# Optimization experiments

Hardware: AMD Instinct MI355X
Metric: run time of the kernel (lower is better)

## Reference

```python
import jax, jax.numpy as jnp
import numpy as np

EMBED = 1024
HEADS = 16
HIDDEN = 4 * EMBED
EPS = 1e-5


def layer_norm(x, g, b):
    mu = jnp.mean(x, axis=-1, keepdims=True)
    var = jnp.var(x, axis=-1, keepdims=True)
    return (x - mu) * jax.lax.rsqrt(var + EPS) * g + b


def setup_inputs() -> dict:
    key = jax.random.key(0)
    ks = jax.random.split(key, 8)
    s = EMBED ** -0.5
    return {
        "x": jax.random.normal(ks[0], (4, 2048, EMBED), dtype=jnp.float32),
        "ln1_g": jnp.ones((EMBED,), jnp.float32),
        "ln1_b": jnp.zeros((EMBED,), jnp.float32),
        "qkv_w": jax.random.normal(ks[1], (3 * EMBED, EMBED), jnp.float32) * s,
        "out_w": jax.random.normal(ks[2], (EMBED, EMBED), jnp.float32) * s,
        "out_b": jnp.zeros((EMBED,), jnp.float32),
        "ln2_g": jnp.ones((EMBED,), jnp.float32),
        "ln2_b": jnp.zeros((EMBED,), jnp.float32),
        "fc1_w": jax.random.normal(ks[3], (HIDDEN, EMBED), jnp.float32) * s,
        "fc1_b": jnp.zeros((HIDDEN,), jnp.float32),
        "fc2_w": jax.random.normal(ks[4], (EMBED, HIDDEN), jnp.float32) * (HIDDEN ** -0.5),
        "fc2_b": jnp.zeros((EMBED,), jnp.float32),
    }


def reference(x, ln1_g, ln1_b, qkv_w, out_w, out_b, ln2_g, ln2_b, fc1_w, fc1_b, fc2_w, fc2_b):
    B, N, C = x.shape
    hd = C // HEADS
    # --- attention (pre-LN); note: NO 1/sqrt(d) scaling, matching the source ---
    h = layer_norm(x, ln1_g, ln1_b)
    qkv = h @ qkv_w.T                                  # [B,N,3C]
    qkv = qkv.reshape(B, N, 3, HEADS, hd).transpose(2, 0, 3, 1, 4)
    q, k, v = qkv[0], qkv[1], qkv[2]                   # [B,H,N,hd]
    attn = jax.nn.softmax(jnp.einsum("bhqd,bhkd->bhqk", q, k), axis=-1)
    o = jnp.einsum("bhqk,bhkd->bhqd", attn, v)
    o = o.transpose(0, 2, 1, 3).reshape(B, N, C)
    x = x + o @ out_w.T + out_b
    # --- MLP (exact erf GELU, matching nn.GELU default) ---
    h = layer_norm(x, ln2_g, ln2_b)
    h = jax.nn.gelu(h @ fc1_w.T + fc1_b, approximate=False)
    x = x + h @ fc2_w.T + fc2_b
    return x
```

## Files before the change

### kernel.cpp

```cpp
#include <hip/hip_runtime.h>
#include <cstdint>


using short8 = __attribute__((ext_vector_type(8))) short;
using f32x4  = __attribute__((ext_vector_type(4))) float;
using f32x16 = __attribute__((ext_vector_type(16))) float;

#define EMBED  1024
#define HIDDEN 4096
#define SEQ    2048
#define NTOK   8192
#define LOG2E  1.4426950408889634f

__device__ __forceinline__ ushort f2bf(float x) {
  union { float f; uint32_t u; } v; v.f = x;
  uint32_t r = v.u + 0x7fffu + ((v.u >> 16) & 1u);
  return (ushort)(r >> 16);
}

__device__ __forceinline__ uint32_t pkbf(float lo, float hi) {
  uint32_t r;
  asm("v_cvt_pk_bf16_f32 %0, %1, %2" : "=v"(r) : "v"(lo), "v"(hi));
  return r;
}

__device__ __forceinline__ void gload16(const void* g, void* l) {
  __builtin_amdgcn_global_load_lds((__attribute__((address_space(1))) void*)(g),
                                   (__attribute__((address_space(3))) void*)(l), 16, 0, 0);
}

template<int N> __device__ __forceinline__ void vwait() {
  asm volatile("s_waitcnt vmcnt(%0)" :: "n"(N) : "memory");
}
__device__ __forceinline__ void lgkm0() {
  asm volatile("s_waitcnt lgkmcnt(0)" ::: "memory");
}
__device__ __forceinline__ void fence_bar() {
  asm volatile("" ::: "memory");
  __builtin_amdgcn_s_barrier();
  asm volatile("" ::: "memory");
}

__device__ __forceinline__ f32x4 mfma16(short8 a, short8 b, f32x4 c) {
  return __builtin_amdgcn_mfma_f32_16x16x32_bf16(a, b, c, 0, 0, 0);
}
__device__ __forceinline__ f32x16 mfma32(short8 a, short8 b, f32x16 c) {
  return __builtin_amdgcn_mfma_f32_32x32x16_bf16(a, b, c, 0, 0, 0);
}
__device__ __forceinline__ f32x16 zero16() {
  f32x16 z = {0.f,0.f,0.f,0.f,0.f,0.f,0.f,0.f,0.f,0.f,0.f,0.f,0.f,0.f,0.f,0.f};
  return z;
}

__global__ __launch_bounds__(256) void cvt4_kernel(const float* __restrict__ s0, ushort* __restrict__ d0, int n0,
                                                   const float* __restrict__ s1, ushort* __restrict__ d1, int n1,
                                                   const float* __restrict__ s2, ushort* __restrict__ d2, int n2,
                                                   const float* __restrict__ s3, ushort* __restrict__ d3, int n3) {
  const int total = n0 + n1 + n2 + n3;
  for (int i = blockIdx.x * 256 + threadIdx.x; i < total; i += gridDim.x * 256) {
    const float* s; ushort* d; int j = i;
    if (j < n0) { s = s0; d = d0; }
    else {
      j -= n0;
      if (j < n1) { s = s1; d = d1; }
      else {
        j -= n1;
        if (j < n2) { s = s2; d = d2; }
        else { j -= n2; s = s3; d = d3; }
      }
    }
    const float4 v = reinterpret_cast<const float4*>(s)[j];
    ushort4 o; o.x = f2bf(v.x); o.y = f2bf(v.y); o.z = f2bf(v.z); o.w = f2bf(v.w);
    reinterpret_cast<ushort4*>(d)[j] = o;
  }
}

__global__ __launch_bounds__(256) void ln_kernel(const float* __restrict__ x,
                                                 const float* __restrict__ g,
                                                 const float* __restrict__ b,
                                                 ushort* __restrict__ out) {
  const int row = blockIdx.x, tid = threadIdx.x;
  const float4 xv = reinterpret_cast<const float4*>(x + (size_t)row * EMBED)[tid];
  float s  = xv.x + xv.y + xv.z + xv.w;
  float s2 = xv.x*xv.x + xv.y*xv.y + xv.z*xv.z + xv.w*xv.w;
  #pragma unroll
  for (int off = 32; off >= 1; off >>= 1) { s += __shfl_xor(s, off); s2 += __shfl_xor(s2, off); }
  __shared__ float ps[4], ps2[4];
  if ((tid & 63) == 0) { ps[tid >> 6] = s; ps2[tid >> 6] = s2; }
  __syncthreads();
  s  = ps[0] + ps[1] + ps[2] + ps[3];
  s2 = ps2[0] + ps2[1] + ps2[2] + ps2[3];
  const float mu  = s * (1.f / EMBED);
  const float var = s2 * (1.f / EMBED) - mu * mu;
  const float rs  = rsqrtf(var + 1e-5f);
  const float4 gv = reinterpret_cast<const float4*>(g)[tid];
  const float4 bv = reinterpret_cast<const float4*>(b)[tid];
  ushort4 o;
  o.x = f2bf((xv.x - mu) * rs * gv.x + bv.x);
  o.y = f2bf((xv.y - mu) * rs * gv.y + bv.y);
  o.z = f2bf((xv.z - mu) * rs * gv.z + bv.z);
  o.w = f2bf((xv.w - mu) * rs * gv.w + bv.w);
  reinterpret_cast<ushort4*>(out + (size_t)row * EMBED)[tid] = o;
}

template<int EPI, bool SQ>
__global__ __launch_bounds__(512) void gemm256(const ushort* __restrict__ A,
                                               const ushort* __restrict__ B,
                                               const float* __restrict__ bias,
                                               const float* __restrict__ res,
                                               ushort* __restrict__ outb,
                                               float* __restrict__ outf,
                                               int M, int N, int K, int gx) {
  constexpr int BN   = SQ ? 256 : 128;
  constexpr int MP   = SQ ? 8 : 4;
  constexpr int NPH  = SQ ? 2 : 1;
  constexpr int LPT  = SQ ? 4 : 3;
  constexpr int NB   = LPT - 2;
  constexpr int ABUF = 256 * 32;
  constexpr int BBUF = BN * 32;
  __shared__ ushort lds[4][ABUF + BBUF];

  const int nwg = gridDim.x;
  const int b0  = blockIdx.x;
  const int p = b0 & 7, li = b0 >> 3;
  int mt, nt;
  if ((gx & 7) == 0) {
    const int g = gx >> 3;
    mt = p * g + (li % g);
    nt = li / g;
  } else {
    const int g = (nwg / gx) >> 3;
    nt = p * g + (li % g);
    mt = li / g;
  }
  const int m0 = mt * 256;
  const int n0 = nt * BN;

  const int tid = threadIdx.x, lane = tid & 63, wave = tid >> 6;
  const int wm = (SQ ? (wave >> 2) : (wave >> 1)) * (MP * 16);
  const int wn = (SQ ? (wave & 3) : (wave & 1)) * 64;
  const int l15 = lane & 15, l4 = lane >> 4;
  const int NT = K >> 5;

  const ushort* aSrc[2];
  const ushort* bSrc[NB];
  #pragma unroll
  for (int rd = 0; rd < 2; ++rd) {
    const int slot = rd * 512 + tid;
    const int r = slot >> 2;
    const int cs = (slot & 3) ^ ((r >> 1) & 3);
    aSrc[rd] = A + (size_t)(m0 + r) * K + cs * 8;
  }
  #pragma unroll
  for (int rd = 0; rd < NB; ++rd) {
    const int slot = rd * 512 + tid;
    const int r = slot >> 2;
    const int cs = (slot & 3) ^ ((r >> 1) & 3);
    bSrc[rd] = B + (size_t)(n0 + r) * K + cs * 8;
  }
  auto stageA = [&](int buf, int rd) { gload16(aSrc[rd], &lds[buf][(rd * 512 + tid) * 8]); };
  auto stageB = [&](int buf, int rd) { gload16(bSrc[rd], &lds[buf][ABUF + (rd * 512 + tid) * 8]); };
  auto advance = [&]() {
    #pragma unroll
    for (int rd = 0; rd < 2; ++rd) aSrc[rd] += 32;
    #pragma unroll
    for (int rd = 0; rd < NB; ++rd) bSrc[rd] += 32;
  };

  #pragma unroll
  for (int t = 0; t < 3; ++t) {
    stageA(t, 0); stageA(t, 1);
    #pragma unroll
    for (int rd = 0; rd < NB; ++rd) stageB(t, rd);
    advance();
  }
  vwait<2 * LPT>();
  fence_bar();

  f32x4 acc[MP][4] = {};

  auto doTile = [&](int q, bool st, int wsel) {
    const ushort* bA = &lds[q][0];
    const ushort* bB = &lds[q][ABUF];
    const int sbuf = (q + 3) & 3;
    short8 bf[4];
    #pragma unroll
    for (int j = 0; j < 4; ++j) {
      const int rb = wn + j * 16 + l15;
      bf[j] = *reinterpret_cast<const short8*>(&bB[rb * 32 + ((l4 ^ ((rb >> 1) & 3)) * 8)]);
    }
    #pragma unroll
    for (int ph = 0; ph < NPH; ++ph) {
      short8 af[4];
      #pragma unroll
      for (int i = 0; i < 4; ++i) {
        const int ra = wm + (ph * 4 + i) * 16 + l15;
        af[i] = *reinterpret_cast<const short8*>(&bA[ra * 32 + ((l4 ^ ((ra >> 1) & 3)) * 8)]);
      }
      if (st) {
        if constexpr (SQ) {
          if (ph == 0) { stageA(sbuf, 0); stageA(sbuf, 1); }
          else         { stageB(sbuf, 0); stageB(sbuf, 1); }
        } else {
          stageA(sbuf, 0); stageA(sbuf, 1); stageB(sbuf, 0);
        }
      }
      fence_bar();
      __builtin_amdgcn_s_setprio(1);
      #pragma unroll
      for (int i = 0; i < 4; ++i)
        #pragma unroll
        for (int j = 0; j < 4; ++j)
          acc[ph * 4 + i][j] = mfma16(af[i], bf[j], acc[ph * 4 + i][j]);
      __builtin_amdgcn_s_setprio(0);
      if (ph == NPH - 1) {
        if (st) advance();
        if (wsel == 0)      vwait<2 * LPT>();
        else if (wsel == 1) vwait<LPT>();
        else if (wsel == 2) vwait<0>();
      }
      fence_bar();
    }
  };

  for (int u0 = 0; u0 < NT - 4; u0 += 4) {
    doTile(0, true, 0); doTile(1, true, 0); doTile(2, true, 0); doTile(3, true, 0);
  }
  doTile(0, true, 0); doTile(1, false, 1); doTile(2, false, 2); doTile(3, false, 3);

  #pragma unroll
  for (int i = 0; i < MP; ++i)
    #pragma unroll
    for (int j = 0; j < 4; ++j)
      #pragma unroll
      for (int r = 0; r < 4; ++r) {
        const int row = m0 + wm + i * 16 + l4 * 4 + r;
        const int col = n0 + wn + j * 16 + l15;
        const size_t idx = (size_t)row * N + col;
        float v = acc[i][j][r];
        if constexpr (EPI == 0) {
          outb[idx] = f2bf(v);
        } else if constexpr (EPI == 1) {
          outf[idx] = v + bias[col] + res[idx];
        } else if constexpr (EPI == 2) {
          v += bias[col];
          v = 0.5f * v * (1.f + erff(v * 0.70710678118654752f));
          outb[idx] = f2bf(v);
        } else {
          outb[idx] = f2bf((col < 1024) ? v * LOG2E : v);
        }
      }
}

#define KVB 64
#define NTT (SEQ / KVB)

__global__ __launch_bounds__(512, 4) void attn_kernel(const ushort* __restrict__ qk,
                                                      const ushort* __restrict__ vt,
                                                      ushort* __restrict__ outp) {
  const int tid = threadIdx.x, lane = tid & 63, wq = tid >> 6;
  const int hi = lane >> 5, lo = lane & 31;
  const int b = blockIdx.x >> 4, h = blockIdx.x & 15;
  const int q0 = blockIdx.y * 256;

  __shared__ ushort sK[2][64 * 64];
  __shared__ ushort sVt[2][64 * 64];
  __shared__ float sBc[8][32];

  short8 qf[4];
  #pragma unroll
  for (int kc = 0; kc < 4; ++kc)
    qf[kc] = *reinterpret_cast<const short8*>(
        qk + (size_t)(b * SEQ + q0 + wq * 32 + lo) * 2048 + h * 64 + kc * 16 + hi * 8);

  auto STAGE = [&](int bb, int kt) {
    const int r = tid >> 3;
    const int c = (tid & 7) ^ (r & 7);
    gload16(qk + (size_t)(b * SEQ + kt + r) * 2048 + 1024 + h * 64 + c * 8,
            &sK[bb][wq * 64 * 8]);
    gload16(vt + (size_t)(h * 64 + r) * 8192 + b * SEQ + kt + c * 8,
            &sVt[bb][wq * 64 * 8]);
  };

  f32x16 acc[2];
  acc[0] = zero16(); acc[1] = zero16();
  float mst = -1e30f, lst = 0.f;

  STAGE(0, 0);
  for (int t = 0; t < NTT; ++t) {
    const int cur = t & 1;
    __syncthreads();
    if (t + 1 < NTT) STAGE(cur ^ 1, (t + 1) * KVB);

    short8 kf[2][4];
    #pragma unroll
    for (int kvb = 0; kvb < 2; ++kvb)
      #pragma unroll
      for (int kc = 0; kc < 4; ++kc) {
        const int row = kvb * 32 + lo, ch = kc * 2 + hi;
        kf[kvb][kc] = *reinterpret_cast<const short8*>(
            &sK[cur][(row * 8 + (ch ^ (row & 7))) * 8]);
      }

    f32x16 st[2];
    #pragma unroll
    for (int kvb = 0; kvb < 2; ++kvb) {
      f32x16 tq = zero16();
      tq = mfma32(kf[kvb][0], qf[0], tq);
      tq = mfma32(kf[kvb][1], qf[1], tq);
      tq = mfma32(kf[kvb][2], qf[2], tq);
      tq = mfma32(kf[kvb][3], qf[3], tq);
      st[kvb] = tq;
    }
    f32x16 mm;
    #pragma unroll
    for (int r = 0; r < 16; ++r) mm[r] = fmaxf(st[0][r], st[1][r]);
    float pm = fmaxf(fmaxf(mm[0], mm[1]), mm[2]);
    pm = fmaxf(fmaxf(pm, mm[3]), mm[4]);
    pm = fmaxf(fmaxf(pm, mm[5]), mm[6]);
    pm = fmaxf(fmaxf(pm, mm[7]), mm[8]);
    pm = fmaxf(fmaxf(pm, mm[9]), mm[10]);
    pm = fmaxf(fmaxf(pm, mm[11]), mm[12]);
    pm = fmaxf(fmaxf(pm, mm[13]), mm[14]);
    pm = fmaxf(pm, mm[15]);
    pm = fmaxf(pm, __shfl_xor(pm, 32));
    if (__any(pm > mst + 11.54f)) {
      const float mn = fmaxf(mst, pm);
      const float al = __builtin_amdgcn_exp2f(mst - mn);
      mst = mn; lst *= al;
      sBc[wq][lo] = al;
      lgkm0();
      #pragma unroll
      for (int g = 0; g < 4; ++g) {
        const f32x4 a4 = *reinterpret_cast<const f32x4*>(&sBc[wq][g * 8 + hi * 4]);
        #pragma unroll
        for (int j = 0; j < 4; ++j) {
          acc[0][g * 4 + j] *= a4[j];
          acc[1][g * 4 + j] *= a4[j];
        }
      }
    }
    #pragma unroll
    for (int kvb = 0; kvb < 2; ++kvb)
      #pragma unroll
      for (int r = 0; r < 16; ++r)
        st[kvb][r] = __builtin_amdgcn_exp2f(st[kvb][r] - mst);
    {
      const f32x16 sv = st[0] + st[1];
      float sum = ((sv[0] + sv[1]) + (sv[2] + sv[3])) + ((sv[4] + sv[5]) + (sv[6] + sv[7]))
                + ((sv[8] + sv[9]) + (sv[10] + sv[11])) + ((sv[12] + sv[13]) + (sv[14] + sv[15]));
      sum += __shfl_xor(sum, 32);
      lst += sum;
    }
    short8 pa[4];
    #pragma unroll
    for (int kvb = 0; kvb < 2; ++kvb)
      #pragma unroll
      for (int f = 0; f < 2; ++f) {
        uint32_t wa = pkbf(st[kvb][f * 8 + 0], st[kvb][f * 8 + 1]);
        uint32_t wb = pkbf(st[kvb][f * 8 + 2], st[kvb][f * 8 + 3]);
        uint32_t wc = pkbf(st[kvb][f * 8 + 4], st[kvb][f * 8 + 5]);
        uint32_t wd = pkbf(st[kvb][f * 8 + 6], st[kvb][f * 8 + 7]);
        asm volatile("v_permlane32_swap_b32 %0, %1" : "+v"(wa), "+v"(wc));
        asm volatile("v_permlane32_swap_b32 %0, %1" : "+v"(wb), "+v"(wd));
        union { uint32_t w[4]; short8 v; } u;
        u.w[0] = wa; u.w[1] = wb; u.w[2] = wc; u.w[3] = wd;
        pa[kvb * 2 + f] = u.v;
      }

    #pragma unroll
    for (int db = 0; db < 2; ++db) {
      short8 vb[4];
      #pragma unroll
      for (int k4 = 0; k4 < 4; ++k4) {
        const int row = db * 32 + lo, ch = k4 * 2 + hi;
        vb[k4] = *reinterpret_cast<const short8*>(
            &sVt[cur][(row * 8 + (ch ^ (row & 7))) * 8]);
      }
      acc[db] = mfma32(pa[0], vb[0], acc[db]);
      acc[db] = mfma32(pa[1], vb[1], acc[db]);
      acc[db] = mfma32(pa[2], vb[2], acc[db]);
      acc[db] = mfma32(pa[3], vb[3], acc[db]);
    }
  }

  sBc[wq][lo] = 1.f / lst;
  lgkm0();
  #pragma unroll
  for (int g = 0; g < 4; ++g) {
    const f32x4 r4 = *reinterpret_cast<const f32x4*>(&sBc[wq][g * 8 + hi * 4]);
    #pragma unroll
    for (int j = 0; j < 4; ++j) {
      const int qrow = q0 + wq * 32 + g * 8 + hi * 4 + j;
      #pragma unroll
      for (int db = 0; db < 2; ++db)
        outp[(size_t)(b * SEQ + qrow) * EMBED + h * 64 + db * 32 + lo] =
            f2bf(acc[db][g * 4 + j] * r4[j]);
    }
  }
}

extern "C" void kernel_launch(void* const* d_in, const int* in_sizes, int n_in,
                              void* d_out, int out_size, void* d_ws, size_t ws_size,
                              hipStream_t stream) {
  const float* x     = (const float*)d_in[0];
  const float* ln1_g = (const float*)d_in[1];
  const float* ln1_b = (const float*)d_in[2];
  const float* qkv_w = (const float*)d_in[3];
  const float* out_w = (const float*)d_in[4];
  const float* out_b = (const float*)d_in[5];
  const float* ln2_g = (const float*)d_in[6];
  const float* ln2_b = (const float*)d_in[7];
  const float* fc1_w = (const float*)d_in[8];
  const float* fc1_b = (const float*)d_in[9];
  const float* fc2_w = (const float*)d_in[10];
  const float* fc2_b = (const float*)d_in[11];
  float* out = (float*)d_out;
  char* ws = (char*)d_ws;

  ushort* qkvw = (ushort*)(ws);
  ushort* outw = (ushort*)(ws + 6291456);
  ushort* fc1w = (ushort*)(ws + 8388608);
  ushort* fc2w = (ushort*)(ws + 16777216);
  float*  x1   = (float*) (ws + 25165824);
  ushort* hbuf = (ushort*)(ws + 58720256);
  ushort* qkbuf= (ushort*)(ws + 75497472);
  ushort* vtbuf= (ushort*)(ws + 109051904);
  ushort* obuf = (ushort*)(ws + 125829120);
  ushort* gbuf = qkbuf;

  cvt4_kernel<<<2048, 256, 0, stream>>>(qkv_w, qkvw, 3 * EMBED * EMBED / 4,
                                        out_w, outw, EMBED * EMBED / 4,
                                        fc1_w, fc1w, HIDDEN * EMBED / 4,
                                        fc2_w, fc2w, EMBED * HIDDEN / 4);

  ln_kernel<<<NTOK, 256, 0, stream>>>(x, ln1_g, ln1_b, hbuf);
  gemm256<3, true><<<256, 512, 0, stream>>>(hbuf, qkvw, nullptr, nullptr,
                                            qkbuf, nullptr, NTOK, 2 * EMBED, EMBED, 32);
  gemm256<0, false><<<256, 512, 0, stream>>>(qkvw + 2048 * 1024, hbuf, nullptr, nullptr,
                                             vtbuf, nullptr, EMBED, NTOK, EMBED, 4);
  attn_kernel<<<dim3(64, 8), 512, 0, stream>>>(qkbuf, vtbuf, obuf);
  gemm256<1, false><<<256, 512, 0, stream>>>(obuf, outw, out_b, x,
                                             nullptr, x1, NTOK, EMBED, EMBED, 32);
  ln_kernel<<<NTOK, 256, 0, stream>>>(x1, ln2_g, ln2_b, hbuf);
  gemm256<2, true><<<512, 512, 0, stream>>>(hbuf, fc1w, fc1_b, nullptr,
                                            gbuf, nullptr, NTOK, HIDDEN, EMBED, 32);
  gemm256<1, false><<<256, 512, 0, stream>>>(gbuf, fc2w, fc2_b, x1,
                                             nullptr, out, NTOK, EMBED, HIDDEN, 32);
}
```

Measured before the change: 379.9 us.

## Switch GEMM to double-buffered LDS and fold LOG2E into Q weights

The GEMM pipeline drops from a 4-stage LDS ring (three tiles in flight, loads issued mid-MFMA) to two buffers, where the next tile's loads are issued after the MFMAs and a barrier. Swizzled LDS offsets are now computed once outside the loop. The LOG2E scaling of Q moves from the QKV GEMM epilogue into the weight-conversion kernel. This halves LDS use, which may allow more resident workgroups, but exposes more global-load latency because less is prefetched and compute overlaps loads less.

```diff
diff --git a/kernel.cpp b/kernel.cpp
--- a/kernel.cpp
+++ b/kernel.cpp
@@ -58,8 +58,8 @@
                                                    const float* __restrict__ s3, ushort* __restrict__ d3, int n3) {
   const int total = n0 + n1 + n2 + n3;
   for (int i = blockIdx.x * 256 + threadIdx.x; i < total; i += gridDim.x * 256) {
-    const float* s; ushort* d; int j = i;
-    if (j < n0) { s = s0; d = d0; }
+    const float* s; ushort* d; int j = i; float sc = 1.f;
+    if (j < n0) { s = s0; d = d0; if (j < (EMBED * EMBED / 4)) sc = LOG2E; }
     else {
       j -= n0;
       if (j < n1) { s = s1; d = d1; }
@@ -70,7 +70,8 @@
       }
     }
     const float4 v = reinterpret_cast<const float4*>(s)[j];
-    ushort4 o; o.x = f2bf(v.x); o.y = f2bf(v.y); o.z = f2bf(v.z); o.w = f2bf(v.w);
+    ushort4 o; o.x = f2bf(v.x * sc); o.y = f2bf(v.y * sc);
+    o.z = f2bf(v.z * sc); o.w = f2bf(v.w * sc);
     reinterpret_cast<ushort4*>(d)[j] = o;
   }
 }
@@ -118,7 +119,7 @@
   constexpr int NB   = LPT - 2;
   constexpr int ABUF = 256 * 32;
   constexpr int BBUF = BN * 32;
-  __shared__ ushort lds[4][ABUF + BBUF];
+  __shared__ ushort lds[2][ABUF + BBUF];
 
   const int nwg = gridDim.x;
   const int b0  = blockIdx.x;
@@ -167,14 +168,26 @@
     for (int rd = 0; rd < NB; ++rd) bSrc[rd] += 32;
   };
 
-  #pragma unroll
-  for (int t = 0; t < 3; ++t) {
+  int aOff[MP], bOff[4];
+  #pragma unroll
+  for (int i = 0; i < MP; ++i) {
+    const int ra = wm + i * 16 + l15;
+    aOff[i] = ra * 32 + ((l4 ^ ((ra >> 1) & 3)) * 8);
+  }
+  #pragma unroll
+  for (int j = 0; j < 4; ++j) {
+    const int rb = wn + j * 16 + l15;
+    bOff[j] = rb * 32 + ((l4 ^ ((rb >> 1) & 3)) * 8);
+  }
+
+  #pragma unroll
+  for (int t = 0; t < 2; ++t) {
     stageA(t, 0); stageA(t, 1);
     #pragma unroll
     for (int rd = 0; rd < NB; ++rd) stageB(t, rd);
     advance();
   }
-  vwait<2 * LPT>();
+  vwait<LPT>();
   fence_bar();
 
   f32x4 acc[MP][4] = {};
@@ -182,30 +195,16 @@
   auto doTile = [&](int q, bool st, int wsel) {
     const ushort* bA = &lds[q][0];
     const ushort* bB = &lds[q][ABUF];
-    const int sbuf = (q + 3) & 3;
     short8 bf[4];
     #pragma unroll
-    for (int j = 0; j < 4; ++j) {
-      const int rb = wn + j * 16 + l15;
-      bf[j] = *reinterpret_cast<const short8*>(&bB[rb * 32 + ((l4 ^ ((rb >> 1) & 3)) * 8)]);
-    }
+    for (int j = 0; j < 4; ++j)
+      bf[j] = *reinterpret_cast<const short8*>(&bB[bOff[j]]);
     #pragma unroll
     for (int ph = 0; ph < NPH; ++ph) {
       short8 af[4];
       #pragma unroll
-      for (int i = 0; i < 4; ++i) {
-        const int ra = wm + (ph * 4 + i) * 16 + l15;
-        af[i] = *reinterpret_cast<const short8*>(&bA[ra * 32 + ((l4 ^ ((ra >> 1) & 3)) * 8)]);
-      }
-      if (st) {
-        if constexpr (SQ) {
-          if (ph == 0) { stageA(sbuf, 0); stageA(sbuf, 1); }
-          else         { stageB(sbuf, 0); stageB(sbuf, 1); }
-        } else {
-          stageA(sbuf, 0); stageA(sbuf, 1); stageB(sbuf, 0);
-        }
-      }
-      fence_bar();
+      for (int i = 0; i < 4; ++i)
+        af[i] = *reinterpret_cast<const short8*>(&bA[aOff[ph * 4 + i]]);
       __builtin_amdgcn_s_setprio(1);
       #pragma unroll
       for (int i = 0; i < 4; ++i)
@@ -213,20 +212,25 @@
         for (int j = 0; j < 4; ++j)
           acc[ph * 4 + i][j] = mfma16(af[i], bf[j], acc[ph * 4 + i][j]);
       __builtin_amdgcn_s_setprio(0);
-      if (ph == NPH - 1) {
-        if (st) advance();
-        if (wsel == 0)      vwait<2 * LPT>();
-        else if (wsel == 1) vwait<LPT>();
-        else if (wsel == 2) vwait<0>();
-      }
-      fence_bar();
-    }
+    }
+    fence_bar();
+    if (st) {
+      stageA(q, 0); stageA(q, 1);
+      #pragma unroll
+      for (int rd = 0; rd < NB; ++rd) stageB(q, rd);
+      advance();
+    }
+    if (wsel == 0)      vwait<LPT>();
+    else if (wsel == 1) vwait<0>();
+    fence_bar();
   };
 
-  for (int u0 = 0; u0 < NT - 4; u0 += 4) {
-    doTile(0, true, 0); doTile(1, true, 0); doTile(2, true, 0); doTile(3, true, 0);
-  }
-  doTile(0, true, 0); doTile(1, false, 1); doTile(2, false, 2); doTile(3, false, 3);
+  for (int u = 0; u < NT - 2; u += 2) {
+    doTile(0, true, 0);
+    doTile(1, (u + 1 < NT - 2), (u + 1 == NT - 2) ? 1 : 0);
+  }
+  doTile(0, false, 1);
+  doTile(1, false, 2);
 
   #pragma unroll
   for (int i = 0; i < MP; ++i)
@@ -242,12 +246,10 @@
           outb[idx] = f2bf(v);
         } else if constexpr (EPI == 1) {
           outf[idx] = v + bias[col] + res[idx];
-        } else if constexpr (EPI == 2) {
+        } else {
           v += bias[col];
           v = 0.5f * v * (1.f + erff(v * 0.70710678118654752f));
           outb[idx] = f2bf(v);
-        } else {
-          outb[idx] = f2bf((col < 1024) ? v * LOG2E : v);
         }
       }
 }
@@ -435,7 +437,7 @@
                                         fc2_w, fc2w, EMBED * HIDDEN / 4);
 
   ln_kernel<<<NTOK, 256, 0, stream>>>(x, ln1_g, ln1_b, hbuf);
-  gemm256<3, true><<<256, 512, 0, stream>>>(hbuf, qkvw, nullptr, nullptr,
+  gemm256<0, true><<<256, 512, 0, stream>>>(hbuf, qkvw, nullptr, nullptr,
                                             qkbuf, nullptr, NTOK, 2 * EMBED, EMBED, 32);
   gemm256<0, false><<<256, 512, 0, stream>>>(qkvw + 2048 * 1024, hbuf, nullptr, nullptr,
                                              vtbuf, nullptr, EMBED, NTOK, EMBED, 4);
```

Measured after the change: 392.0 us. +3.2%, slower.
